# Performance work log

Hardware: AMD Instinct MI355X
Metric: run time of the kernel (lower is better)

## Reference

```python
import jax, jax.numpy as jnp
import numpy as np

IN_F = 4096
OUT_F = 4096
BATCH = 256


def setup_inputs() -> dict:
    key = jax.random.key(0)
    ks = jax.random.split(key, 5)
    stdv = 1.0 / np.sqrt(IN_F)
    x = jax.random.normal(ks[0], (BATCH, IN_F), dtype=jnp.float32)
    weight_mu = jax.random.uniform(ks[1], (OUT_F, IN_F), dtype=jnp.float32, minval=-stdv, maxval=stdv)
    bias_mu = jax.random.uniform(ks[2], (OUT_F,), dtype=jnp.float32, minval=-stdv, maxval=stdv)
    weight_logvar = jnp.full((OUT_F, IN_F), -6.0, dtype=jnp.float32)
    bias_logvar = jnp.full((OUT_F,), -6.0, dtype=jnp.float32)
    weight_eps = jax.random.normal(ks[3], (OUT_F, IN_F), dtype=jnp.float32)
    bias_eps = jax.random.normal(ks[4], (OUT_F,), dtype=jnp.float32)
    return {
        "x": x,
        "weight_mu": weight_mu,
        "weight_logvar": weight_logvar,
        "bias_mu": bias_mu,
        "bias_logvar": bias_logvar,
        "weight_eps": weight_eps,
        "bias_eps": bias_eps,
    }


def reference(x, weight_mu, weight_logvar, bias_mu, bias_logvar, weight_eps, bias_eps):
    # Reparameterized sample: W = mu + eps * exp(0.5 * logvar)
    weight = weight_mu + weight_eps * jnp.exp(0.5 * weight_logvar)   # [O, I]
    bias = bias_mu + bias_eps * jnp.exp(0.5 * bias_logvar)           # [O]
    # F.linear: y = x @ W^T + b
    return jnp.einsum('bi,oi->bo', x, weight) + bias
```

## Files before the change

### kernel.cpp

```cpp
#include <hip/hip_runtime.h>
#include <stdint.h>
#include <stddef.h>

#define BATCH 256
#define IN_F  4096
#define OUT_F 4096
#define BN    16
#define BK    64
#define KSPLIT 4
#define TPB   256

#define RAW_BUF   12288
#define RAW_ARR   4096
#define BF_BASE   24576
#define LDS_TOTAL 26624

typedef __attribute__((ext_vector_type(8))) short    bf16x8;
typedef __attribute__((ext_vector_type(4))) float    f32x4;
typedef __attribute__((ext_vector_type(2))) uint32_t u32x2;
typedef __attribute__((ext_vector_type(4))) uint32_t u32x4;

#define MFMA(a,b,c) __builtin_amdgcn_mfma_f32_16x16x32_bf16((a),(b),(c),0,0,0)
#define HALF_LOG2E 0.7213475204444817f

__device__ __forceinline__ uint32_t pack2bf(float a, float b) {
  uint32_t ua = __builtin_bit_cast(uint32_t, a);
  uint32_t ub = __builtin_bit_cast(uint32_t, b);
  ua += 0x7FFFu + ((ua >> 16) & 1u);
  ub += 0x7FFFu + ((ub >> 16) & 1u);
  return (ua >> 16) | (ub & 0xFFFF0000u);
}

__device__ __forceinline__ bf16x8 cvt8(const float* p) {
  f32x4 v0 = *(const f32x4*)p;
  f32x4 v1 = *(const f32x4*)(p + 4);
  union { u32x4 u; bf16x8 h; } r;
  r.u[0] = pack2bf(v0[0], v0[1]); r.u[1] = pack2bf(v0[2], v0[3]);
  r.u[2] = pack2bf(v1[0], v1[1]); r.u[3] = pack2bf(v1[2], v1[3]);
  return r.h;
}

__device__ __forceinline__ void gload_lds16(const void* g, void* l) {
  __builtin_amdgcn_global_load_lds(
      (const __attribute__((address_space(1))) uint32_t*)g,
      (__attribute__((address_space(3))) uint32_t*)l, 16, 0, 0);
}

__global__ __launch_bounds__(256) void prep_kernel(
    const float* __restrict__ x,
    const float* __restrict__ bmu,
    const float* __restrict__ blv,
    const float* __restrict__ beps,
    u32x4* __restrict__ xs4,
    float* __restrict__ bias)
{
  const uint32_t b = blockIdx.x;
  if (b < 512u) {
    const uint32_t c = b * 256u + threadIdx.x;
    const float* p = x + (size_t)c * 8u;
    f32x4 v0 = *(const f32x4*)p;
    f32x4 v1 = *(const f32x4*)(p + 4);
    u32x4 o;
    o[0] = pack2bf(v0[0], v0[1]); o[1] = pack2bf(v0[2], v0[3]);
    o[2] = pack2bf(v1[0], v1[1]); o[3] = pack2bf(v1[2], v1[3]);
    xs4[c] = o;
  } else {
    const uint32_t i = (b - 512u) * 256u + threadIdx.x;
    bias[i] = fmaf(beps[i], exp2f(blv[i] * HALF_LOG2E), bmu[i]);
  }
}

template<int NSPLIT, bool USE_XS>
__global__ __launch_bounds__(TPB, 4)
void vgemm(const uint16_t* __restrict__ xs,
           const float*    __restrict__ xf,
           const float*    __restrict__ wmu,
           const float*    __restrict__ wlv,
           const float*    __restrict__ weps,
           const float*    __restrict__ biasp,
           const float*    __restrict__ bmu,
           const float*    __restrict__ blv,
           const float*    __restrict__ beps,
           float*          __restrict__ out)
{
  __shared__ __align__(16) uint8_t lds[LDS_TOTAL];

  const int tid = threadIdx.x;
  const int wv  = tid >> 6;
  const int l   = tid & 63;
  const int col_tile = blockIdx.x / NSPLIT;
  const int ks       = blockIdx.x % NSPLIT;
  const int n0  = col_tile * BN;
  const int k0  = ks * (IN_F / NSPLIT);
  const int NT  = (IN_F / NSPLIT) / BK;

  const size_t sgoff = (size_t)(n0 + 4 * wv + (l >> 4)) * IN_F + k0 + ((l & 15) << 2);

  const int cr = tid >> 4;
  const int ci = tid & 15;
  const int bfw = cr * 128 + ((((ci >> 1) ^ (cr & 7)) << 4)) + ((ci & 1) << 3);

  const int br = l & 15;
  const int kb = l >> 4;
  const int bfo0 = br * 128 + ((((0 * 4 + kb)) ^ (br & 7)) << 4);
  const int bfo1 = br * 128 + ((((1 * 4 + kb)) ^ (br & 7)) << 4);
  const int arow0 = wv * 64 + br;

  f32x4 acc[4] = {{0,0,0,0},{0,0,0,0},{0,0,0,0},{0,0,0,0}};

  auto STAGE = [&](int t, int buf) {
    const size_t go = sgoff + (size_t)t * BK;
    uint8_t* base = &lds[0] + buf * RAW_BUF + wv * 1024;
    gload_lds16(wmu  + go, base + 0 * RAW_ARR);
    gload_lds16(wlv  + go, base + 1 * RAW_ARR);
    gload_lds16(weps + go, base + 2 * RAW_ARR);
  };

  auto CVT = [&](int buf) {
    const uint8_t* rb = &lds[0] + buf * RAW_BUF;
    f32x4 m = *(const f32x4*)(rb + 0 * RAW_ARR + tid * 16);
    f32x4 v = *(const f32x4*)(rb + 1 * RAW_ARR + tid * 16);
    f32x4 e = *(const f32x4*)(rb + 2 * RAW_ARR + tid * 16);
    u32x2 o;
    o[0] = pack2bf(fmaf(e[0], exp2f(v[0] * HALF_LOG2E), m[0]),
                   fmaf(e[1], exp2f(v[1] * HALF_LOG2E), m[1]));
    o[1] = pack2bf(fmaf(e[2], exp2f(v[2] * HALF_LOG2E), m[2]),
                   fmaf(e[3], exp2f(v[3] * HALF_LOG2E), m[3]));
    *(u32x2*)(&lds[0] + BF_BASE + bfw) = o;
  };

  auto COMP = [&](int t) {
    const uint8_t* bfb = &lds[0] + BF_BASE;
    bf16x8 b0 = *(const bf16x8*)(bfb + bfo0);
    bf16x8 b1 = *(const bf16x8*)(bfb + bfo1);
    const size_t kb0 = (size_t)k0 + t * BK + kb * 8;
#pragma unroll
    for (int j = 0; j < 4; ++j) {
      bf16x8 a0, a1;
      if constexpr (USE_XS) {
        const uint16_t* xp = xs + (size_t)(arow0 + 16 * j) * IN_F + kb0;
        a0 = *(const bf16x8*)(xp);
        a1 = *(const bf16x8*)(xp + 32);
      } else {
        const float* xp = xf + (size_t)(arow0 + 16 * j) * IN_F + kb0;
        a0 = cvt8(xp);
        a1 = cvt8(xp + 32);
      }
      acc[j] = MFMA(a0, b0, acc[j]);
      acc[j] = MFMA(a1, b1, acc[j]);
    }
  };

  STAGE(0, 0);
  for (int t = 0; t < NT; ++t) {
    if (t + 1 < NT) STAGE(t + 1, (t + 1) & 1);
    __syncthreads();
    CVT(t & 1);
    __syncthreads();
    COMP(t);
  }

  const int col = n0 + br;
  if constexpr (NSPLIT == 1) {
    float bv;
    if constexpr (USE_XS) bv = biasp[col];
    else bv = fmaf(beps[col], exp2f(blv[col] * HALF_LOG2E), bmu[col]);
#pragma unroll
    for (int j = 0; j < 4; ++j) {
      const int rbase = wv * 64 + j * 16 + kb * 4;
#pragma unroll
      for (int i = 0; i < 4; ++i)
        out[(size_t)(rbase + i) * OUT_F + col] = acc[j][i] + bv;
    }
  } else {
    float* po = out + (size_t)ks * BATCH * OUT_F;
#pragma unroll
    for (int j = 0; j < 4; ++j) {
      const int rbase = wv * 64 + j * 16 + kb * 4;
#pragma unroll
      for (int i = 0; i < 4; ++i)
        po[(size_t)(rbase + i) * OUT_F + col] = acc[j][i];
    }
  }
}

__global__ __launch_bounds__(256) void reduce_kernel(
    const float* __restrict__ parts,
    const float* __restrict__ bias,
    float* __restrict__ y)
{
  const size_t e = ((size_t)blockIdx.x * 256 + threadIdx.x) * 4;
  f32x4 s = *(const f32x4*)(parts + e);
#pragma unroll
  for (int p = 1; p < KSPLIT; ++p)
    s += *(const f32x4*)(parts + (size_t)p * BATCH * OUT_F + e);
  s += *(const f32x4*)(bias + (e & (OUT_F - 1)));
  *(f32x4*)(y + e) = s;
}

extern "C" void kernel_launch(void* const* d_in, const int* in_sizes, int n_in,
                              void* d_out, int out_size, void* d_ws, size_t ws_size,
                              hipStream_t stream) {
  const float* x    = (const float*)d_in[0];
  const float* wmu  = (const float*)d_in[1];
  const float* wlv  = (const float*)d_in[2];
  const float* bmu  = (const float*)d_in[3];
  const float* blv  = (const float*)d_in[4];
  const float* weps = (const float*)d_in[5];
  const float* beps = (const float*)d_in[6];
  float* y = (float*)d_out;

  const size_t xs_b   = (size_t)BATCH * IN_F * 2;
  const size_t bias_b = (size_t)OUT_F * 4;
  const size_t part_b = (size_t)KSPLIT * BATCH * OUT_F * 4;

  if (d_ws != nullptr && ws_size >= xs_b + bias_b + part_b) {
    uint16_t* xsp   = (uint16_t*)d_ws;
    float*    bias  = (float*)((char*)d_ws + xs_b);
    float*    parts = (float*)((char*)d_ws + xs_b + bias_b);
    prep_kernel<<<528, 256, 0, stream>>>(x, bmu, blv, beps, (u32x4*)d_ws, bias);
    vgemm<KSPLIT, true><<<(OUT_F / BN) * KSPLIT, TPB, 0, stream>>>(
        xsp, nullptr, wmu, wlv, weps, bias, nullptr, nullptr, nullptr, parts);
    reduce_kernel<<<(BATCH * OUT_F) / (256 * 4), 256, 0, stream>>>(parts, bias, y);
  } else if (d_ws != nullptr && ws_size >= xs_b + bias_b) {
    uint16_t* xsp  = (uint16_t*)d_ws;
    float*    bias = (float*)((char*)d_ws + xs_b);
    prep_kernel<<<528, 256, 0, stream>>>(x, bmu, blv, beps, (u32x4*)d_ws, bias);
    vgemm<1, true><<<OUT_F / BN, TPB, 0, stream>>>(
        xsp, nullptr, wmu, wlv, weps, bias, nullptr, nullptr, nullptr, y);
  } else {
    vgemm<1, false><<<OUT_F / BN, TPB, 0, stream>>>(
        nullptr, x, wmu, wlv, weps, nullptr, bmu, blv, beps, y);
  }
}
```

Before: 83.29 us.

## Precompute sampled weights into swizzled bf16 tile image before GEMM

Adds a separate weight-conversion kernel that samples W = mu + eps*exp(0.5*logvar) once and writes it as bf16 in a pre-swizzled, tile-contiguous layout. A new GEMM kernel then streams that image straight into LDS with direct global-to-LDS loads, with no per-tile conversion pass and one fewer barrier per iteration. It also widens each block to 32 output columns so each x fragment feeds two weight tiles. The cost is an extra full pass that writes and rereads a 32 MB bf16 weight image and needs a larger workspace. If the workspace is too small, it falls back to the old path.

After: 85.55 us. 2.7% more time.

```diff
diff --git a/kernel.cpp b/kernel.cpp
--- a/kernel.cpp
+++ b/kernel.cpp
@@ -5,15 +5,7 @@
 #define BATCH 256
 #define IN_F  4096
 #define OUT_F 4096
-#define BN    16
-#define BK    64
 #define KSPLIT 4
-#define TPB   256
-
-#define RAW_BUF   12288
-#define RAW_ARR   4096
-#define BF_BASE   24576
-#define LDS_TOTAL 26624
 
 typedef __attribute__((ext_vector_type(8))) short    bf16x8;
 typedef __attribute__((ext_vector_type(4))) float    f32x4;
@@ -70,18 +62,142 @@
   }
 }
 
+__global__ __launch_bounds__(256) void wcvt_kernel(
+    const float* __restrict__ wmu,
+    const float* __restrict__ wlv,
+    const float* __restrict__ weps,
+    uint8_t* __restrict__ wimg)
+{
+  const uint32_t c = blockIdx.x * 256u + threadIdx.x;
+  const uint32_t n = c >> 9;
+  const uint32_t q = c & 511u;
+  const size_t  off = ((size_t)n << 12) + (q << 3);
+  f32x4 m0 = *(const f32x4*)(wmu + off);
+  f32x4 m1 = *(const f32x4*)(wmu + off + 4);
+  f32x4 v0 = *(const f32x4*)(wlv + off);
+  f32x4 v1 = *(const f32x4*)(wlv + off + 4);
+  f32x4 e0 = *(const f32x4*)(weps + off);
+  f32x4 e1 = *(const f32x4*)(weps + off + 4);
+  u32x4 o;
+  o[0] = pack2bf(fmaf(e0[0], exp2f(v0[0] * HALF_LOG2E), m0[0]),
+                 fmaf(e0[1], exp2f(v0[1] * HALF_LOG2E), m0[1]));
+  o[1] = pack2bf(fmaf(e0[2], exp2f(v0[2] * HALF_LOG2E), m0[2]),
+                 fmaf(e0[3], exp2f(v0[3] * HALF_LOG2E), m0[3]));
+  o[2] = pack2bf(fmaf(e1[0], exp2f(v1[0] * HALF_LOG2E), m1[0]),
+                 fmaf(e1[1], exp2f(v1[1] * HALF_LOG2E), m1[1]));
+  o[3] = pack2bf(fmaf(e1[2], exp2f(v1[2] * HALF_LOG2E), m1[2]),
+                 fmaf(e1[3], exp2f(v1[3] * HALF_LOG2E), m1[3]));
+  const uint32_t nt = n >> 4, r = n & 15u, kt = q >> 4, g = q & 15u;
+  *(u32x4*)(wimg + (((size_t)(nt * 32u + kt)) << 12)
+                 + (r << 8) + (((g ^ r) & 15u) << 4)) = o;
+}
+
+template<int NSPLIT>
+__global__ __launch_bounds__(256, 2)
+void vgemm_img(const uint16_t* __restrict__ xs,
+               const uint8_t*  __restrict__ wimg,
+               const float*    __restrict__ biasp,
+               float*          __restrict__ out)
+{
+  __shared__ __align__(16) uint8_t lds[16384];
+
+  const int tid = threadIdx.x;
+  const int wv  = tid >> 6;
+  const int l   = tid & 63;
+  const int cg  = blockIdx.x / NSPLIT;
+  const int ks  = blockIdx.x % NSPLIT;
+  const int nt0 = cg * 2;
+  const int KT0 = ks * (32 / NSPLIT);
+  const int NIT = 32 / NSPLIT;
+
+  const int br = l & 15;
+  const int kb = l >> 4;
+  const int arow0 = wv * 64 + br;
+
+  f32x4 acc0[4] = {{0,0,0,0},{0,0,0,0},{0,0,0,0},{0,0,0,0}};
+  f32x4 acc1[4] = {{0,0,0,0},{0,0,0,0},{0,0,0,0},{0,0,0,0}};
+
+  auto STAGE = [&](int t, int buf) {
+    const int kt = KT0 + t;
+#pragma unroll
+    for (int j = 0; j < 2; ++j) {
+      const int ch = wv * 2 + j;
+      const int i  = ch >> 2;
+      const int q  = ch & 3;
+      const uint8_t* src = wimg + (((size_t)((nt0 + i) * 32 + kt)) << 12)
+                                + q * 1024 + l * 16;
+      gload_lds16(src, &lds[0] + buf * 8192 + i * 4096 + q * 1024 + l * 16);
+    }
+  };
+
+  auto COMP = [&](int t, int buf) {
+    const uint8_t* B = &lds[0] + buf * 8192;
+#pragma unroll
+    for (int s = 0; s < 4; ++s) {
+      const int swz = br * 256 + ((((s * 4 + kb) ^ br) & 15) << 4);
+      bf16x8 b0 = *(const bf16x8*)(B + swz);
+      bf16x8 b1 = *(const bf16x8*)(B + 4096 + swz);
+      const size_t kk = (size_t)(KT0 + t) * 128 + s * 32 + kb * 8;
+#pragma unroll
+      for (int j = 0; j < 4; ++j) {
+        bf16x8 a = *(const bf16x8*)(xs + (size_t)(arow0 + 16 * j) * IN_F + kk);
+        acc0[j] = MFMA(a, b0, acc0[j]);
+        acc1[j] = MFMA(a, b1, acc1[j]);
+      }
+    }
+  };
+
+  STAGE(0, 0);
+  for (int t = 0; t < NIT; ++t) {
+    if (t + 1 < NIT) STAGE(t + 1, (t + 1) & 1);
+    __syncthreads();
+    COMP(t, t & 1);
+    __syncthreads();
+  }
+
+#pragma unroll
+  for (int img = 0; img < 2; ++img) {
+    const f32x4* acc = img ? acc1 : acc0;
+    const int col = cg * 32 + img * 16 + br;
+    if constexpr (NSPLIT == 1) {
+      const float bv = biasp[col];
+#pragma unroll
+      for (int j = 0; j < 4; ++j) {
+        const int rbase = wv * 64 + j * 16 + kb * 4;
+#pragma unroll
+        for (int i = 0; i < 4; ++i)
+          out[(size_t)(rbase + i) * OUT_F + col] = acc[j][i] + bv;
+      }
+    } else {
+      float* po = out + (size_t)ks * BATCH * OUT_F;
+#pragma unroll
+      for (int j = 0; j < 4; ++j) {
+        const int rbase = wv * 64 + j * 16 + kb * 4;
+#pragma unroll
+        for (int i = 0; i < 4; ++i)
+          po[(size_t)(rbase + i) * OUT_F + col] = acc[j][i];
+      }
+    }
+  }
+}
+
+#define RAW_BUF   12288
+#define RAW_ARR   4096
+#define BF_BASE   24576
+#define LDS_TOTAL 26624
+
 template<int NSPLIT, bool USE_XS>
-__global__ __launch_bounds__(TPB, 4)
-void vgemm(const uint16_t* __restrict__ xs,
-           const float*    __restrict__ xf,
-           const float*    __restrict__ wmu,
-           const float*    __restrict__ wlv,
-           const float*    __restrict__ weps,
-           const float*    __restrict__ biasp,
-           const float*    __restrict__ bmu,
-           const float*    __restrict__ blv,
-           const float*    __restrict__ beps,
-           float*          __restrict__ out)
+__global__ __launch_bounds__(256, 4)
+void vgemm3(const uint16_t* __restrict__ xs,
+            const float*    __restrict__ xf,
+            const float*    __restrict__ wmu,
+            const float*    __restrict__ wlv,
+            const float*    __restrict__ weps,
+            const float*    __restrict__ biasp,
+            const float*    __restrict__ bmu,
+            const float*    __restrict__ blv,
+            const float*    __restrict__ beps,
+            float*          __restrict__ out)
 {
   __shared__ __align__(16) uint8_t lds[LDS_TOTAL];
 
@@ -90,16 +206,14 @@
   const int l   = tid & 63;
   const int col_tile = blockIdx.x / NSPLIT;
   const int ks       = blockIdx.x % NSPLIT;
-  const int n0  = col_tile * BN;
+  const int n0  = col_tile * 16;
   const int k0  = ks * (IN_F / NSPLIT);
-  const int NT  = (IN_F / NSPLIT) / BK;
+  const int NT  = (IN_F / NSPLIT) / 64;
 
   const size_t sgoff = (size_t)(n0 + 4 * wv + (l >> 4)) * IN_F + k0 + ((l & 15) << 2);
-
   const int cr = tid >> 4;
   const int ci = tid & 15;
   const int bfw = cr * 128 + ((((ci >> 1) ^ (cr & 7)) << 4)) + ((ci & 1) << 3);
-
   const int br = l & 15;
   const int kb = l >> 4;
   const int bfo0 = br * 128 + ((((0 * 4 + kb)) ^ (br & 7)) << 4);
@@ -109,13 +223,12 @@
   f32x4 acc[4] = {{0,0,0,0},{0,0,0,0},{0,0,0,0},{0,0,0,0}};
 
   auto STAGE = [&](int t, int buf) {
-    const size_t go = sgoff + (size_t)t * BK;
+    const size_t go = sgoff + (size_t)t * 64;
     uint8_t* base = &lds[0] + buf * RAW_BUF + wv * 1024;
     gload_lds16(wmu  + go, base + 0 * RAW_ARR);
     gload_lds16(wlv  + go, base + 1 * RAW_ARR);
     gload_lds16(weps + go, base + 2 * RAW_ARR);
   };
-
   auto CVT = [&](int buf) {
     const uint8_t* rb = &lds[0] + buf * RAW_BUF;
     f32x4 m = *(const f32x4*)(rb + 0 * RAW_ARR + tid * 16);
@@ -128,12 +241,11 @@
                    fmaf(e[3], exp2f(v[3] * HALF_LOG2E), m[3]));
     *(u32x2*)(&lds[0] + BF_BASE + bfw) = o;
   };
-
   auto COMP = [&](int t) {
     const uint8_t* bfb = &lds[0] + BF_BASE;
     bf16x8 b0 = *(const bf16x8*)(bfb + bfo0);
     bf16x8 b1 = *(const bf16x8*)(bfb + bfo1);
-    const size_t kb0 = (size_t)k0 + t * BK + kb * 8;
+    const size_t kb0 = (size_t)k0 + t * 64 + kb * 8;
 #pragma unroll
     for (int j = 0; j < 4; ++j) {
       bf16x8 a0, a1;
@@ -213,23 +325,35 @@
   const size_t xs_b   = (size_t)BATCH * IN_F * 2;
   const size_t bias_b = (size_t)OUT_F * 4;
   const size_t part_b = (size_t)KSPLIT * BATCH * OUT_F * 4;
-
-  if (d_ws != nullptr && ws_size >= xs_b + bias_b + part_b) {
-    uint16_t* xsp   = (uint16_t*)d_ws;
-    float*    bias  = (float*)((char*)d_ws + xs_b);
-    float*    parts = (float*)((char*)d_ws + xs_b + bias_b);
+  const size_t img_b  = (size_t)OUT_F * IN_F * 2;
+
+  uint16_t* xsp  = (uint16_t*)d_ws;
+  float*    bias = (float*)((char*)d_ws + xs_b);
+
+  if (d_ws && ws_size >= xs_b + bias_b + part_b + img_b) {
+    float*   parts = (float*)((char*)d_ws + xs_b + bias_b);
+    uint8_t* wimg  = (uint8_t*)d_ws + xs_b + bias_b + part_b;
     prep_kernel<<<528, 256, 0, stream>>>(x, bmu, blv, beps, (u32x4*)d_ws, bias);
-    vgemm<KSPLIT, true><<<(OUT_F / BN) * KSPLIT, TPB, 0, stream>>>(
+    wcvt_kernel<<<8192, 256, 0, stream>>>(wmu, wlv, weps, wimg);
+    vgemm_img<KSPLIT><<<(OUT_F / 32) * KSPLIT, 256, 0, stream>>>(xsp, wimg, bias, parts);
+    reduce_kernel<<<(BATCH * OUT_F) / (256 * 4), 256, 0, stream>>>(parts, bias, y);
+  } else if (d_ws && ws_size >= xs_b + bias_b + img_b) {
+    uint8_t* wimg = (uint8_t*)d_ws + xs_b + bias_b;
+    prep_kernel<<<528, 256, 0, stream>>>(x, bmu, blv, beps, (u32x4*)d_ws, bias);
+    wcvt_kernel<<<8192, 256, 0, stream>>>(wmu, wlv, weps, wimg);
+    vgemm_img<1><<<OUT_F / 32, 256, 0, stream>>>(xsp, wimg, bias, y);
+  } else if (d_ws && ws_size >= xs_b + bias_b + part_b) {
+    float* parts = (float*)((char*)d_ws + xs_b + bias_b);
+    prep_kernel<<<528, 256, 0, stream>>>(x, bmu, blv, beps, (u32x4*)d_ws, bias);
+    vgemm3<KSPLIT, true><<<(OUT_F / 16) * KSPLIT, 256, 0, stream>>>(
         xsp, nullptr, wmu, wlv, weps, bias, nullptr, nullptr, nullptr, parts);
     reduce_kernel<<<(BATCH * OUT_F) / (256 * 4), 256, 0, stream>>>(parts, bias, y);
-  } else if (d_ws != nullptr && ws_size >= xs_b + bias_b) {
-    uint16_t* xsp  = (uint16_t*)d_ws;
-    float*    bias = (float*)((char*)d_ws + xs_b);
+  } else if (d_ws && ws_size >= xs_b + bias_b) {
     prep_kernel<<<528, 256, 0, stream>>>(x, bmu, blv, beps, (u32x4*)d_ws, bias);
-    vgemm<1, true><<<OUT_F / BN, TPB, 0, stream>>>(
+    vgemm3<1, true><<<OUT_F / 16, 256, 0, stream>>>(
         xsp, nullptr, wmu, wlv, weps, bias, nullptr, nullptr, nullptr, y);
   } else {
-    vgemm<1, false><<<OUT_F / BN, TPB, 0, stream>>>(
+    vgemm3<1, false><<<OUT_F / 16, 256, 0, stream>>>(
         nullptr, x, wmu, wlv, weps, nullptr, bmu, blv, beps, y);
   }
 }
```

## Prefetch weight tiles into registers instead of staging raw fp32 through LDS

Applied to the files above, without the earlier changes.

The main GEMM kernel now loads the mu/logvar/eps weight tiles straight into registers with nontemporal loads, one tile ahead, and writes only the converted bf16 tile to a small double-buffered LDS area. This drops the raw fp32 LDS staging and one of the two barriers per K step, and shrinks LDS use. The x conversion loads in the prep kernel also become nontemporal. The cost is more live registers per thread and reliance on register prefetch depth to hide HBM latency in place of async global-to-LDS copies.

Result: slower. 94.91 us (+13.9%).

```diff
diff --git a/kernel.cpp b/kernel.cpp
--- a/kernel.cpp
+++ b/kernel.cpp
@@ -5,15 +5,7 @@
 #define BATCH 256
 #define IN_F  4096
 #define OUT_F 4096
-#define BN    16
-#define BK    64
 #define KSPLIT 4
-#define TPB   256
-
-#define RAW_BUF   12288
-#define RAW_ARR   4096
-#define BF_BASE   24576
-#define LDS_TOTAL 26624
 
 typedef __attribute__((ext_vector_type(8))) short    bf16x8;
 typedef __attribute__((ext_vector_type(4))) float    f32x4;
@@ -22,6 +14,7 @@
 
 #define MFMA(a,b,c) __builtin_amdgcn_mfma_f32_16x16x32_bf16((a),(b),(c),0,0,0)
 #define HALF_LOG2E 0.7213475204444817f
+#define HLG HALF_LOG2E
 
 __device__ __forceinline__ uint32_t pack2bf(float a, float b) {
   uint32_t ua = __builtin_bit_cast(uint32_t, a);
@@ -44,6 +37,10 @@
   __builtin_amdgcn_global_load_lds(
       (const __attribute__((address_space(1))) uint32_t*)g,
       (__attribute__((address_space(3))) uint32_t*)l, 16, 0, 0);
+}
+
+__device__ __forceinline__ f32x4 ntld4(const float* p) {
+  return __builtin_nontemporal_load((const f32x4*)p);
 }
 
 __global__ __launch_bounds__(256) void prep_kernel(
@@ -58,43 +55,39 @@
   if (b < 512u) {
     const uint32_t c = b * 256u + threadIdx.x;
     const float* p = x + (size_t)c * 8u;
-    f32x4 v0 = *(const f32x4*)p;
-    f32x4 v1 = *(const f32x4*)(p + 4);
+    f32x4 v0 = ntld4(p);
+    f32x4 v1 = ntld4(p + 4);
     u32x4 o;
     o[0] = pack2bf(v0[0], v0[1]); o[1] = pack2bf(v0[2], v0[3]);
     o[2] = pack2bf(v1[0], v1[1]); o[3] = pack2bf(v1[2], v1[3]);
     xs4[c] = o;
   } else {
     const uint32_t i = (b - 512u) * 256u + threadIdx.x;
-    bias[i] = fmaf(beps[i], exp2f(blv[i] * HALF_LOG2E), bmu[i]);
-  }
-}
-
-template<int NSPLIT, bool USE_XS>
-__global__ __launch_bounds__(TPB, 4)
-void vgemm(const uint16_t* __restrict__ xs,
-           const float*    __restrict__ xf,
-           const float*    __restrict__ wmu,
-           const float*    __restrict__ wlv,
-           const float*    __restrict__ weps,
-           const float*    __restrict__ biasp,
-           const float*    __restrict__ bmu,
-           const float*    __restrict__ blv,
-           const float*    __restrict__ beps,
-           float*          __restrict__ out)
+    bias[i] = fmaf(beps[i], exp2f(blv[i] * HLG), bmu[i]);
+  }
+}
+
+template<int NSPLIT>
+__global__ __launch_bounds__(256, 4)
+void vgemm_fused(const uint16_t* __restrict__ xs,
+                 const float*    __restrict__ wmu,
+                 const float*    __restrict__ wlv,
+                 const float*    __restrict__ weps,
+                 const float*    __restrict__ biasp,
+                 float*          __restrict__ out)
 {
-  __shared__ __align__(16) uint8_t lds[LDS_TOTAL];
+  __shared__ __align__(16) uint8_t bfl[2][2048];
 
   const int tid = threadIdx.x;
   const int wv  = tid >> 6;
   const int l   = tid & 63;
   const int col_tile = blockIdx.x / NSPLIT;
   const int ks       = blockIdx.x % NSPLIT;
-  const int n0  = col_tile * BN;
+  const int n0  = col_tile * 16;
   const int k0  = ks * (IN_F / NSPLIT);
-  const int NT  = (IN_F / NSPLIT) / BK;
-
-  const size_t sgoff = (size_t)(n0 + 4 * wv + (l >> 4)) * IN_F + k0 + ((l & 15) << 2);
+  const int NT  = (IN_F / NSPLIT) / 64;
+
+  const size_t wbase = (size_t)(n0 + (tid >> 4)) * IN_F + k0 + ((tid & 15) << 2);
 
   const int cr = tid >> 4;
   const int ci = tid & 15;
@@ -108,32 +101,159 @@
 
   f32x4 acc[4] = {{0,0,0,0},{0,0,0,0},{0,0,0,0},{0,0,0,0}};
 
+  f32x4 mA, vA, eA, mB, vB, eB;
+
+#define WLOADS(M,V,E,t) do {                         \
+    const size_t _o = wbase + (size_t)(t) * 64;      \
+    M = ntld4(wmu + _o);                             \
+    V = ntld4(wlv + _o);                             \
+    E = ntld4(weps + _o);                            \
+  } while (0)
+
+#define WCVT(buf, M, V, E) do {                                       \
+    u32x2 _o;                                                         \
+    _o[0] = pack2bf(fmaf(E[0], exp2f(V[0]*HLG), M[0]),                \
+                    fmaf(E[1], exp2f(V[1]*HLG), M[1]));               \
+    _o[1] = pack2bf(fmaf(E[2], exp2f(V[2]*HLG), M[2]),                \
+                    fmaf(E[3], exp2f(V[3]*HLG), M[3]));               \
+    *(u32x2*)(&bfl[buf][bfw]) = _o;                                   \
+  } while (0)
+
+  auto COMP = [&](int t, int buf) {
+    bf16x8 b0 = *(const bf16x8*)(&bfl[buf][bfo0]);
+    bf16x8 b1 = *(const bf16x8*)(&bfl[buf][bfo1]);
+    const size_t kk = (size_t)k0 + (size_t)t * 64 + kb * 8;
+#pragma unroll
+    for (int j = 0; j < 4; ++j) {
+      const uint16_t* xp = xs + (size_t)(arow0 + 16 * j) * IN_F + kk;
+      bf16x8 a0 = *(const bf16x8*)(xp);
+      bf16x8 a1 = *(const bf16x8*)(xp + 32);
+      acc[j] = MFMA(a0, b0, acc[j]);
+      acc[j] = MFMA(a1, b1, acc[j]);
+    }
+  };
+
+  WLOADS(mA, vA, eA, 0);
+  for (int t = 0; t < NT; t += 2) {
+    {
+      if (t + 1 < NT) WLOADS(mB, vB, eB, t + 1);
+      WCVT(0, mA, vA, eA);
+      asm volatile("s_waitcnt lgkmcnt(0)" ::: "memory");
+      __builtin_amdgcn_s_barrier();
+      COMP(t, 0);
+    }
+    {
+      if (t + 2 < NT) WLOADS(mA, vA, eA, t + 2);
+      WCVT(1, mB, vB, eB);
+      asm volatile("s_waitcnt lgkmcnt(0)" ::: "memory");
+      __builtin_amdgcn_s_barrier();
+      COMP(t + 1, 1);
+    }
+  }
+#undef WLOADS
+#undef WCVT
+
+  const int col = n0 + br;
+  if constexpr (NSPLIT == 1) {
+    const float bv = biasp[col];
+#pragma unroll
+    for (int j = 0; j < 4; ++j) {
+      const int rbase = wv * 64 + j * 16 + kb * 4;
+#pragma unroll
+      for (int i = 0; i < 4; ++i)
+        out[(size_t)(rbase + i) * OUT_F + col] = acc[j][i] + bv;
+    }
+  } else {
+    float* po = out + (size_t)ks * BATCH * OUT_F;
+#pragma unroll
+    for (int j = 0; j < 4; ++j) {
+      const int rbase = wv * 64 + j * 16 + kb * 4;
+#pragma unroll
+      for (int i = 0; i < 4; ++i)
+        po[(size_t)(rbase + i) * OUT_F + col] = acc[j][i];
+    }
+  }
+}
+
+__global__ __launch_bounds__(256) void reduce_kernel(
+    const float* __restrict__ parts,
+    const float* __restrict__ bias,
+    float* __restrict__ y)
+{
+  const size_t e = ((size_t)blockIdx.x * 256 + threadIdx.x) * 4;
+  f32x4 s = *(const f32x4*)(parts + e);
+#pragma unroll
+  for (int p = 1; p < KSPLIT; ++p)
+    s += *(const f32x4*)(parts + (size_t)p * BATCH * OUT_F + e);
+  s += *(const f32x4*)(bias + (e & (OUT_F - 1)));
+  *(f32x4*)(y + e) = s;
+}
+
+#define RAW_BUF   12288
+#define RAW_ARR   4096
+#define BF_BASE   24576
+#define LDS_TOTAL 26624
+
+template<int NSPLIT, bool USE_XS>
+__global__ __launch_bounds__(256, 4)
+void vgemm3(const uint16_t* __restrict__ xs,
+            const float*    __restrict__ xf,
+            const float*    __restrict__ wmu,
+            const float*    __restrict__ wlv,
+            const float*    __restrict__ weps,
+            const float*    __restrict__ biasp,
+            const float*    __restrict__ bmu,
+            const float*    __restrict__ blv,
+            const float*    __restrict__ beps,
+            float*          __restrict__ out)
+{
+  __shared__ __align__(16) uint8_t lds[LDS_TOTAL];
+
+  const int tid = threadIdx.x;
+  const int wv  = tid >> 6;
+  const int l   = tid & 63;
+  const int col_tile = blockIdx.x / NSPLIT;
+  const int ks       = blockIdx.x % NSPLIT;
+  const int n0  = col_tile * 16;
+  const int k0  = ks * (IN_F / NSPLIT);
+  const int NT  = (IN_F / NSPLIT) / 64;
+
+  const size_t sgoff = (size_t)(n0 + 4 * wv + (l >> 4)) * IN_F + k0 + ((l & 15) << 2);
+  const int cr = tid >> 4;
+  const int ci = tid & 15;
+  const int bfw = cr * 128 + ((((ci >> 1) ^ (cr & 7)) << 4)) + ((ci & 1) << 3);
+  const int br = l & 15;
+  const int kb = l >> 4;
+  const int bfo0 = br * 128 + ((((0 * 4 + kb)) ^ (br & 7)) << 4);
+  const int bfo1 = br * 128 + ((((1 * 4 + kb)) ^ (br & 7)) << 4);
+  const int arow0 = wv * 64 + br;
+
+  f32x4 acc[4] = {{0,0,0,0},{0,0,0,0},{0,0,0,0},{0,0,0,0}};
+
   auto STAGE = [&](int t, int buf) {
-    const size_t go = sgoff + (size_t)t * BK;
+    const size_t go = sgoff + (size_t)t * 64;
     uint8_t* base = &lds[0] + buf * RAW_BUF + wv * 1024;
     gload_lds16(wmu  + go, base + 0 * RAW_ARR);
     gload_lds16(wlv  + go, base + 1 * RAW_ARR);
     gload_lds16(weps + go, base + 2 * RAW_ARR);
   };
-
   auto CVT = [&](int buf) {
     const uint8_t* rb = &lds[0] + buf * RAW_BUF;
     f32x4 m = *(const f32x4*)(rb + 0 * RAW_ARR + tid * 16);
     f32x4 v = *(const f32x4*)(rb + 1 * RAW_ARR + tid * 16);
     f32x4 e = *(const f32x4*)(rb + 2 * RAW_ARR + tid * 16);
     u32x2 o;
-    o[0] = pack2bf(fmaf(e[0], exp2f(v[0] * HALF_LOG2E), m[0]),
-                   fmaf(e[1], exp2f(v[1] * HALF_LOG2E), m[1]));
-    o[1] = pack2bf(fmaf(e[2], exp2f(v[2] * HALF_LOG2E), m[2]),
-                   fmaf(e[3], exp2f(v[3] * HALF_LOG2E), m[3]));
+    o[0] = pack2bf(fmaf(e[0], exp2f(v[0] * HLG), m[0]),
+                   fmaf(e[1], exp2f(v[1] * HLG), m[1]));
+    o[1] = pack2bf(fmaf(e[2], exp2f(v[2] * HLG), m[2]),
+                   fmaf(e[3], exp2f(v[3] * HLG), m[3]));
     *(u32x2*)(&lds[0] + BF_BASE + bfw) = o;
   };
-
   auto COMP = [&](int t) {
     const uint8_t* bfb = &lds[0] + BF_BASE;
     bf16x8 b0 = *(const bf16x8*)(bfb + bfo0);
     bf16x8 b1 = *(const bf16x8*)(bfb + bfo1);
-    const size_t kb0 = (size_t)k0 + t * BK + kb * 8;
+    const size_t kb0 = (size_t)k0 + t * 64 + kb * 8;
 #pragma unroll
     for (int j = 0; j < 4; ++j) {
       bf16x8 a0, a1;
@@ -164,7 +284,7 @@
   if constexpr (NSPLIT == 1) {
     float bv;
     if constexpr (USE_XS) bv = biasp[col];
-    else bv = fmaf(beps[col], exp2f(blv[col] * HALF_LOG2E), bmu[col]);
+    else bv = fmaf(beps[col], exp2f(blv[col] * HLG), bmu[col]);
 #pragma unroll
     for (int j = 0; j < 4; ++j) {
       const int rbase = wv * 64 + j * 16 + kb * 4;
@@ -182,20 +302,6 @@
         po[(size_t)(rbase + i) * OUT_F + col] = acc[j][i];
     }
   }
-}
-
-__global__ __launch_bounds__(256) void reduce_kernel(
-    const float* __restrict__ parts,
-    const float* __restrict__ bias,
-    float* __restrict__ y)
-{
-  const size_t e = ((size_t)blockIdx.x * 256 + threadIdx.x) * 4;
-  f32x4 s = *(const f32x4*)(parts + e);
-#pragma unroll
-  for (int p = 1; p < KSPLIT; ++p)
-    s += *(const f32x4*)(parts + (size_t)p * BATCH * OUT_F + e);
-  s += *(const f32x4*)(bias + (e & (OUT_F - 1)));
-  *(f32x4*)(y + e) = s;
 }
 
 extern "C" void kernel_launch(void* const* d_in, const int* in_sizes, int n_in,
@@ -214,22 +320,21 @@
   const size_t bias_b = (size_t)OUT_F * 4;
   const size_t part_b = (size_t)KSPLIT * BATCH * OUT_F * 4;
 
-  if (d_ws != nullptr && ws_size >= xs_b + bias_b + part_b) {
-    uint16_t* xsp   = (uint16_t*)d_ws;
-    float*    bias  = (float*)((char*)d_ws + xs_b);
-    float*    parts = (float*)((char*)d_ws + xs_b + bias_b);
+  uint16_t* xsp  = (uint16_t*)d_ws;
+  float*    bias = (float*)((char*)d_ws + xs_b);
+
+  if (d_ws && ws_size >= xs_b + bias_b + part_b) {
+    float* parts = (float*)((char*)d_ws + xs_b + bias_b);
     prep_kernel<<<528, 256, 0, stream>>>(x, bmu, blv, beps, (u32x4*)d_ws, bias);
-    vgemm<KSPLIT, true><<<(OUT_F / BN) * KSPLIT, TPB, 0, stream>>>(
-        xsp, nullptr, wmu, wlv, weps, bias, nullptr, nullptr, nullptr, parts);
+    vgemm_fused<KSPLIT><<<(OUT_F / 16) * KSPLIT, 256, 0, stream>>>(
+        xsp, wmu, wlv, weps, bias, parts);
     reduce_kernel<<<(BATCH * OUT_F) / (256 * 4), 256, 0, stream>>>(parts, bias, y);
-  } else if (d_ws != nullptr && ws_size >= xs_b + bias_b) {
-    uint16_t* xsp  = (uint16_t*)d_ws;
-    float*    bias = (float*)((char*)d_ws + xs_b);
+  } else if (d_ws && ws_size >= xs_b + bias_b) {
     prep_kernel<<<528, 256, 0, stream>>>(x, bmu, blv, beps, (u32x4*)d_ws, bias);
-    vgemm<1, true><<<OUT_F / BN, TPB, 0, stream>>>(
-        xsp, nullptr, wmu, wlv, weps, bias, nullptr, nullptr, nullptr, y);
+    vgemm_fused<1><<<OUT_F / 16, 256, 0, stream>>>(
+        xsp, wmu, wlv, weps, bias, y);
   } else {
-    vgemm<1, false><<<OUT_F / BN, TPB, 0, stream>>>(
+    vgemm3<1, false><<<OUT_F / 16, 256, 0, stream>>>(
         nullptr, x, wmu, wlv, weps, nullptr, bmu, blv, beps, y);
   }
 }
```
